# Kernel optimization log

Measured on AMD Instinct MI355X. Metric: run time of the kernel, lower is better.

## Reference

```python
import jax, jax.numpy as jnp
import numpy as np

N_NODES = 10000
N_EDGES = 640000
F_IN = 128
HID = 128
N_LAYERS = 3
N_ACT = 4096
NEG_SLOPE = 0.2


def setup_inputs() -> dict:
    key = jax.random.key(0)
    ks = jax.random.split(key, 16)
    s = 0.05
    return {
        "x": jax.random.normal(ks[0], (N_NODES, F_IN), jnp.float32),
        "edge_index": jax.random.randint(ks[1], (2, N_EDGES), 0, N_NODES, jnp.int64),
        "action_src": jax.random.randint(ks[2], (N_ACT,), 0, N_NODES, jnp.int64),
        "action_dst": jax.random.randint(ks[3], (N_ACT,), 0, N_NODES, jnp.int64),
        "action_type": jax.random.randint(ks[4], (N_ACT,), 0, 2, jnp.int32),
        "gat_W": jax.random.normal(ks[5], (N_LAYERS, HID, HID), jnp.float32) * s,
        "gat_asrc": jax.random.normal(ks[6], (N_LAYERS, HID), jnp.float32) * s,
        "gat_adst": jax.random.normal(ks[7], (N_LAYERS, HID), jnp.float32) * s,
        "gat_b": jax.random.normal(ks[8], (N_LAYERS, HID), jnp.float32) * s,
        "mlp_W1": jax.random.normal(ks[9], (2 * HID + 1, HID), jnp.float32) * s,
        "mlp_b1": jax.random.normal(ks[10], (HID,), jnp.float32) * s,
        "mlp_W2": jax.random.normal(ks[11], (HID, 1), jnp.float32) * s,
        "mlp_b2": jax.random.normal(ks[12], (1,), jnp.float32) * s,
    }


def _gat_layer(h, src, dst, W, a_src, a_dst, b, n_nodes):
    # PyG GATConv, heads=1: z = h W; e_ij = leaky_relu(a_src.z_j + a_dst.z_i)
    z = h @ W                                   # [N, HID]
    e = jax.nn.leaky_relu((z @ a_src)[src] + (z @ a_dst)[dst], NEG_SLOPE)  # [E+N]
    m = jax.ops.segment_max(e, dst, num_segments=n_nodes)
    m = jnp.where(jnp.isfinite(m), m, 0.0)
    ex = jnp.exp(e - m[dst])
    denom = jax.ops.segment_sum(ex, dst, num_segments=n_nodes)
    alpha = ex / denom[dst]                     # softmax over incoming edges
    out = jax.ops.segment_sum(alpha[:, None] * z[src], dst, num_segments=n_nodes)
    return out + b


def reference(x, edge_index, action_src, action_dst, action_type,
              gat_W, gat_asrc, gat_adst, gat_b,
              mlp_W1, mlp_b1, mlp_W2, mlp_b2):
    n = x.shape[0]
    loop = jnp.arange(n, dtype=edge_index.dtype)  # add_self_loops=True
    src = jnp.concatenate([edge_index[0], loop])
    dst = jnp.concatenate([edge_index[1], loop])
    h = x
    for l in range(N_LAYERS):
        h = jax.nn.relu(_gat_layer(h, src, dst, gat_W[l], gat_asrc[l], gat_adst[l], gat_b[l], n))
    # vectorized action scoring: [h[src], h[dst], type_flag] -> MLP -> scalar
    feat = jnp.concatenate(
        [h[action_src], h[action_dst], action_type.astype(h.dtype)[:, None]], axis=-1)
    hidden = jax.nn.relu(feat @ mlp_W1 + mlp_b1)
    scores = (hidden @ mlp_W2 + mlp_b2)[:, 0]   # [N_ACT]
    return scores
```

## Files before the change

### kernel.cpp

```cpp
#include <hip/hip_runtime.h>
#include <hip/hip_bf16.h>
#include <hip/hip_fp16.h>

#define N_NODES 10000
#define N_EDGES 640000
#define TOT_E   (N_EDGES + N_NODES)
#define HID     128
#define NEG_SLOPE 0.2f
#define N_ACT   4096

#define NBKT   250
#define NPB    40
#define P1_EPB 4096
#define P1_EPT 16
#define P1_BLOCKS 159
#define SLOTP  56
#define G_BLOCKS 313

__global__ __launch_bounds__(256) void part1_k(const int* __restrict__ ei,
                                               unsigned* __restrict__ bpart,
                                               int* __restrict__ bcnt) {
    __shared__ int hist[256];
    __shared__ int lofs[256];
    __shared__ int sc[256];
    __shared__ unsigned stage[P1_EPB];
    __shared__ unsigned char bkt_of[P1_EPB];
    int t = threadIdx.x;
    hist[t] = 0;
    __syncthreads();

    unsigned pk[P1_EPT];
    int bk[P1_EPT];
    int e0 = blockIdx.x * P1_EPB;
#pragma unroll
    for (int i = 0; i < P1_EPT; i++) {
        int e = e0 + i * 256 + t;
        if (e < TOT_E) {
            int src, dst;
            if (e < N_EDGES) { src = ei[e]; dst = ei[N_EDGES + e]; }
            else             { src = e - N_EDGES; dst = src; }
            pk[i] = ((unsigned)dst << 16) | (unsigned)src;
            bk[i] = dst / NPB;
            atomicAdd(&hist[bk[i]], 1);
        } else bk[i] = -1;
    }
    __syncthreads();
    int v = hist[t];
    sc[t] = v;
    __syncthreads();
    for (int o = 1; o < 256; o <<= 1) {
        int u = (t >= o) ? sc[t - o] : 0;
        __syncthreads();
        sc[t] += u;
        __syncthreads();
    }
    lofs[t] = sc[t] - v;
    bcnt[blockIdx.x * 256 + t] = v;
    hist[t] = 0;
    __syncthreads();
#pragma unroll
    for (int i = 0; i < P1_EPT; i++) {
        if (bk[i] >= 0) {
            int p = atomicAdd(&hist[bk[i]], 1);
            int slot = lofs[bk[i]] + p;
            stage[slot] = pk[i];
            bkt_of[slot] = (unsigned char)bk[i];
        }
    }
    __syncthreads();
    int nv = min(P1_EPB, TOT_E - e0);
    for (int s = t; s < nv; s += 256) {
        int b = bkt_of[s];
        bpart[b * (P1_BLOCKS * SLOTP) + blockIdx.x * SLOTP + (s - lofs[b])] = stage[s];
    }
}

__device__ __forceinline__ void agg_node(const __half2* __restrict__ z2,
                                         const float* __restrict__ zsi, float zdn,
                                         const int* __restrict__ csr, int o0, int deg,
                                         int lane, float& accx, float& accy, float& denom) {
    for (int base = 0; base < deg; base += 64) {
        int j = base + lane;
        int sreg = 0;
        float ex = 0.f;
        if (j < deg) {
            int s = csr[o0 + j];
            sreg = s;
            float e = zsi[s] + zdn;
            e = e > 0.f ? e : NEG_SLOPE * e;
            ex = __expf(e);
        }
        int cnt = min(64, deg - base);
        int nfull = cnt & ~7;
        int q = 0;
        if (nfull) {
            __half2 cur[8];
            float exc[8];
#pragma unroll
            for (int u = 0; u < 8; u++) {
                int sq = __builtin_amdgcn_readlane(sreg, u);
                exc[u] = __uint_as_float(
                    __builtin_amdgcn_readlane(__float_as_uint(ex), u));
                cur[u] = z2[sq * 64];
            }
            for (q = 8; q < nfull; q += 8) {
                __half2 nxt[8];
                float exn[8];
#pragma unroll
                for (int u = 0; u < 8; u++) {
                    int sq = __builtin_amdgcn_readlane(sreg, q + u);
                    exn[u] = __uint_as_float(
                        __builtin_amdgcn_readlane(__float_as_uint(ex), q + u));
                    nxt[u] = z2[sq * 64];
                }
#pragma unroll
                for (int u = 0; u < 8; u++) {
                    denom += exc[u];
                    float2 vf = __half22float2(cur[u]);
                    accx = fmaf(exc[u], vf.x, accx);
                    accy = fmaf(exc[u], vf.y, accy);
                    cur[u] = nxt[u];
                    exc[u] = exn[u];
                }
            }
#pragma unroll
            for (int u = 0; u < 8; u++) {
                denom += exc[u];
                float2 vf = __half22float2(cur[u]);
                accx = fmaf(exc[u], vf.x, accx);
                accy = fmaf(exc[u], vf.y, accy);
            }
            q = nfull;
        }
        for (; q < cnt; q++) {
            int sq = __builtin_amdgcn_readlane(sreg, q);
            float exq = __uint_as_float(
                __builtin_amdgcn_readlane(__float_as_uint(ex), q));
            denom += exq;
            float2 vf = __half22float2(z2[sq * 64]);
            accx = fmaf(exq, vf.x, accx);
            accy = fmaf(exq, vf.y, accy);
        }
    }
}

__device__ __forceinline__ void gload_lds16(const float* g, float* l) {
    __builtin_amdgcn_global_load_lds(
        (const __attribute__((address_space(1))) void*)g,
        (__attribute__((address_space(3))) void*)l, 16, 0, 0);
}

__global__ __launch_bounds__(256) void g2_k(const float* __restrict__ A,
                                            const float* __restrict__ W,
                                            const float* __restrict__ avs,
                                            const float* __restrict__ avd,
                                            __half* __restrict__ z16,
                                            float* __restrict__ zs,
                                            float* __restrict__ zd,
                                            const unsigned* __restrict__ bpart,
                                            const int* __restrict__ bcnt,
                                            int* __restrict__ csr,
                                            int* __restrict__ offs) {
    __shared__ float smem[20480];
    int t = threadIdx.x;

    if (blockIdx.x < G_BLOCKS) {
        float* As = smem;
        float* Ws = smem + 32 * HID;
        int w = t >> 6, lane = t & 63;
        int row0 = blockIdx.x * 32;
#pragma unroll
        for (int i = 0; i < 4; i++) {
            int chunk = w * 4 + i;
            long foff = (long)row0 * HID + chunk * 256;
            const float* g = ((foff + 256) <= (long)N_NODES * HID) ? (A + foff + lane * 4)
                                                                   : (A + lane * 4);
            gload_lds16(g, As + chunk * 256);
        }
#pragma unroll
        for (int i = 0; i < 16; i++) {
            int chunk = w * 16 + i;
            gload_lds16(W + chunk * 256 + lane * 4, Ws + chunk * 256);
        }
        __syncthreads();

        int tx = t & 31, ty = t >> 5;
        int r0 = ty * 4;
        float acc[4][4] = {{0.f}};
#pragma unroll 4
        for (int k4 = 0; k4 < 32; k4++) {
            float ak[4][4];
#pragma unroll
            for (int r = 0; r < 4; r++) {
                float4 a4 = *(const float4*)&As[(r0 + r) * HID + k4 * 4];
                ak[r][0] = a4.x; ak[r][1] = a4.y; ak[r][2] = a4.z; ak[r][3] = a4.w;
            }
            const float* Wb = &Ws[k4 * 4 * HID + tx * 4];
#pragma unroll
            for (int kk = 0; kk < 4; kk++) {
                float4 wv = *(const float4*)&Wb[kk * HID];
#pragma unroll
                for (int r = 0; r < 4; r++) {
                    acc[r][0] = fmaf(ak[r][kk], wv.x, acc[r][0]);
                    acc[r][1] = fmaf(ak[r][kk], wv.y, acc[r][1]);
                    acc[r][2] = fmaf(ak[r][kk], wv.z, acc[r][2]);
                    acc[r][3] = fmaf(ak[r][kk], wv.w, acc[r][3]);
                }
            }
        }
        float4 asv = *(const float4*)&avs[tx * 4];
        float4 adv = *(const float4*)&avd[tx * 4];
#pragma unroll
        for (int r = 0; r < 4; r++) {
            int row = row0 + r0 + r;
            if (row < N_NODES) {
                *(__half2*)&z16[row * HID + tx * 4]     = __floats2half2_rn(acc[r][0], acc[r][1]);
                *(__half2*)&z16[row * HID + tx * 4 + 2] = __floats2half2_rn(acc[r][2], acc[r][3]);
            }
            float ps = acc[r][0] * asv.x + acc[r][1] * asv.y + acc[r][2] * asv.z + acc[r][3] * asv.w;
            float pd = acc[r][0] * adv.x + acc[r][1] * adv.y + acc[r][2] * adv.z + acc[r][3] * adv.w;
#pragma unroll
            for (int o = 1; o < 32; o <<= 1) {
                ps += __shfl_xor(ps, o, 64);
                pd += __shfl_xor(pd, o, 64);
            }
            if (tx == 0 && row < N_NODES) { zs[row] = ps; zd[row] = pd; }
        }
    } else {
        int b = blockIdx.x - G_BLOCKS;
        unsigned* ebuf = (unsigned*)smem;
        int* sc    = (int*)(smem + 4096);
        int* Ls    = sc + 256;
        int* nhist = Ls + 256;
        __shared__ int bstart_s, cnt_s;

        int tot = 0;
        if (t < NBKT) {
            int t0 = 0, t1 = 0, t2 = 0, t3 = 0;
            int blk = 0;
            for (; blk + 4 <= P1_BLOCKS; blk += 4) {
                t0 += bcnt[(blk + 0) * 256 + t];
                t1 += bcnt[(blk + 1) * 256 + t];
                t2 += bcnt[(blk + 2) * 256 + t];
                t3 += bcnt[(blk + 3) * 256 + t];
            }
            for (; blk < P1_BLOCKS; blk++) t0 += bcnt[blk * 256 + t];
            tot = t0 + t1 + t2 + t3;
        }
        sc[t] = tot;
        __syncthreads();
        for (int o = 1; o < 256; o <<= 1) {
            int u = (t >= o) ? sc[t - o] : 0;
            __syncthreads();
            sc[t] += u;
            __syncthreads();
        }
        if (t == b) { bstart_s = sc[t] - tot; cnt_s = tot; }
        if (b == 0 && t == 255) offs[N_NODES] = sc[255];
        __syncthreads();

        int L = (t < P1_BLOCKS) ? bcnt[t * 256 + b] : 0;
        Ls[t] = L;
        sc[t] = L;
        __syncthreads();
        for (int o = 1; o < 256; o <<= 1) {
            int u = (t >= o) ? sc[t - o] : 0;
            __syncthreads();
            sc[t] += u;
            __syncthreads();
        }
        if (t < NPB) nhist[t] = 0;
        {
            int wv = t >> 6, lane = t & 63;
            const unsigned* bbase = bpart + b * (P1_BLOCKS * SLOTP);
            for (int r = wv; r < P1_BLOCKS; r += 4) {
                int Lr = Ls[r];
                if (lane < Lr) ebuf[(sc[r] - Lr) + lane] = bbase[r * SLOTP + lane];
            }
        }
        __syncthreads();

        int cnt = cnt_s;
        int n0 = b * NPB;
        for (int i = t; i < cnt; i += 256) atomicAdd(&nhist[(ebuf[i] >> 16) - n0], 1);
        __syncthreads();
        if (t < 64) {
            int v2 = (t < NPB) ? nhist[t] : 0;
            int s2 = v2;
            for (int o = 1; o < 64; o <<= 1) {
                int u = __shfl_up(s2, o, 64);
                if (t >= o) s2 += u;
            }
            if (t < NPB) {
                int ofs = bstart_s + s2 - v2;
                nhist[t] = ofs;
                offs[n0 + t] = ofs;
            }
        }
        __syncthreads();
        for (int i = t; i < cnt; i += 256) {
            unsigned pk = ebuf[i];
            int p = atomicAdd(&nhist[(pk >> 16) - n0], 1);
            csr[p] = pk & 0xFFFF;
        }
    }
}


__global__ __launch_bounds__(256) void fuse_k(const __half* __restrict__ z16i,
                                              const float* __restrict__ zsi,
                                              const float* __restrict__ zdi,
                                              const int* __restrict__ offs,
                                              const int* __restrict__ csr,
                                              const float* __restrict__ bprev,
                                              const float* __restrict__ W,
                                              const float* __restrict__ avs,
                                              const float* __restrict__ avd,
                                              __half* __restrict__ z16o,
                                              float* __restrict__ zso,
                                              float* __restrict__ zdo) {
    __shared__ float hT[8][HID];
    __shared__ float Wc[2][32 * HID];
    int t = threadIdx.x;
    int w = t >> 6, lane = t & 63;
    int n0 = blockIdx.x * 8;
    float4 wreg[4];
    {
        const float4* Wg = (const float4*)W;
#pragma unroll
        for (int i = 0; i < 4; i++) wreg[i] = Wg[t + 256 * i];
    }
    const __half2* z2 = (const __half2*)z16i + lane;

    float2 bv = *(const float2*)&bprev[2 * lane];
#pragma unroll
    for (int i = 0; i < 2; i++) {
        int ln = w * 2 + i;
        int n = n0 + ln;
        int o0 = offs[n];
        int deg = offs[n + 1] - o0;
        float zdn = zdi[n];
        float accx = 0.f, accy = 0.f, denom = 0.f;
        agg_node(z2, zsi, zdn, csr, o0, deg, lane, accx, accy, denom);
        float inv = 1.0f / denom;
        float vx = accx * inv + bv.x;
        float vy = accy * inv + bv.y;
        float2 hv;
        hv.x = vx > 0.f ? vx : 0.f;
        hv.y = vy > 0.f ? vy : 0.f;
        *(float2*)&hT[ln][2 * lane] = hv;
    }

    int tx = t & 31, ty = t >> 5;
    float acc[4] = {0.f, 0.f, 0.f, 0.f};
    for (int c = 0; c < 4; c++) {
        float4* dstb = (float4*)Wc[c & 1];
#pragma unroll
        for (int i = 0; i < 4; i++) dstb[t + 256 * i] = wreg[i];
        __syncthreads();
        if (c + 1 < 4) {
            const float4* Wg = (const float4*)(W + (c + 1) * 32 * HID);
#pragma unroll
            for (int i = 0; i < 4; i++) wreg[i] = Wg[t + 256 * i];
        }
        const float* Wb = Wc[c & 1];
        const float* h0 = &hT[ty][c * 32];
#pragma unroll 8
        for (int kk = 0; kk < 32; kk++) {
            float f0 = h0[kk];
            float4 wv = *(const float4*)&Wb[kk * HID + tx * 4];
            acc[0] = fmaf(f0, wv.x, acc[0]);
            acc[1] = fmaf(f0, wv.y, acc[1]);
            acc[2] = fmaf(f0, wv.z, acc[2]);
            acc[3] = fmaf(f0, wv.w, acc[3]);
        }
    }
    float4 asv = *(const float4*)&avs[tx * 4];
    float4 adv = *(const float4*)&avd[tx * 4];
    int row = n0 + ty;
    *(__half2*)&z16o[row * HID + tx * 4]     = __floats2half2_rn(acc[0], acc[1]);
    *(__half2*)&z16o[row * HID + tx * 4 + 2] = __floats2half2_rn(acc[2], acc[3]);
    float ps = acc[0] * asv.x + acc[1] * asv.y + acc[2] * asv.z + acc[3] * asv.w;
    float pd = acc[0] * adv.x + acc[1] * adv.y + acc[2] * adv.z + acc[3] * adv.w;
#pragma unroll
    for (int o = 1; o < 32; o <<= 1) {
        ps += __shfl_xor(ps, o, 64);
        pd += __shfl_xor(pd, o, 64);
    }
    if (tx == 0) { zso[row] = ps; zdo[row] = pd; }
}


__global__ __launch_bounds__(256) void agg_k(const __half* __restrict__ z16,
                                             const float* __restrict__ zs,
                                             const float* __restrict__ zd,
                                             const int* __restrict__ offs,
                                             const int* __restrict__ csr,
                                             const float* __restrict__ b,
                                             float* __restrict__ hout) {
    int t = threadIdx.x;
    int w = t >> 6, lane = t & 63;
    int n = blockIdx.x * 4 + w;
    if (n >= N_NODES) return;
    int o0 = offs[n];
    int deg = offs[n + 1] - o0;
    float zdn = zd[n];
    const __half2* z2 = (const __half2*)z16 + lane;
    float accx = 0.f, accy = 0.f, denom = 0.f;
    agg_node(z2, zs, zdn, csr, o0, deg, lane, accx, accy, denom);
    float inv = 1.0f / denom;
    float2 bv = *(const float2*)&b[2 * lane];
    float vx = accx * inv + bv.x;
    float vy = accy * inv + bv.y;
    float2 o;
    o.x = vx > 0.f ? vx : 0.f;
    o.y = vy > 0.f ? vy : 0.f;
    *(float2*)&hout[n * HID + 2 * lane] = o;
}


#define SC_APB 16

__global__ __launch_bounds__(256) void score_k(const float* __restrict__ h,
                                               const int* __restrict__ asrc,
                                               const int* __restrict__ adst,
                                               const int* __restrict__ atype,
                                               const float* __restrict__ W1,
                                               const float* __restrict__ b1,
                                               const float* __restrict__ W2,
                                               const float* __restrict__ b2,
                                               float* __restrict__ out) {
    __shared__ float featT[257][SC_APB + 1];
    __shared__ float Wc[2][32 * HID];
    int t = threadIdx.x;
    int a0 = blockIdx.x * SC_APB;

    float4 wreg[4];
    {
        const float4* Wg = (const float4*)W1;
#pragma unroll
        for (int i = 0; i < 4; i++) wreg[i] = Wg[t + 256 * i];
    }
    for (int idx = t; idx < SC_APB * 128; idx += 256) {
        int a = idx >> 7, c = idx & 127;
        featT[c][a]       = h[asrc[a0 + a] * HID + c];
        featT[128 + c][a] = h[adst[a0 + a] * HID + c];
    }
    if (t < SC_APB) featT[256][t] = (float)atype[a0 + t];

    int cg = t & 31, ap = t >> 5;
    float4 bv = *(const float4*)&b1[cg * 4];
    float acc0[4] = {bv.x, bv.y, bv.z, bv.w};
    float acc1[4] = {bv.x, bv.y, bv.z, bv.w};

    for (int c = 0; c < 8; c++) {
        float4* dstb = (float4*)Wc[c & 1];
#pragma unroll
        for (int i = 0; i < 4; i++) dstb[t + 256 * i] = wreg[i];
        __syncthreads();
        if (c + 1 < 8) {
            const float4* Wg = (const float4*)(W1 + (c + 1) * 32 * HID);
#pragma unroll
            for (int i = 0; i < 4; i++) wreg[i] = Wg[t + 256 * i];
        }
        const float* Wb = Wc[c & 1];
        const float* fT = &featT[c * 32][0];
#pragma unroll 8
        for (int kk = 0; kk < 32; kk++) {
            float4 wv = *(const float4*)&Wb[kk * HID + cg * 4];
            float f0 = fT[kk * (SC_APB + 1) + ap * 2];
            float f1 = fT[kk * (SC_APB + 1) + ap * 2 + 1];
            acc0[0] = fmaf(f0, wv.x, acc0[0]);
            acc0[1] = fmaf(f0, wv.y, acc0[1]);
            acc0[2] = fmaf(f0, wv.z, acc0[2]);
            acc0[3] = fmaf(f0, wv.w, acc0[3]);
            acc1[0] = fmaf(f1, wv.x, acc1[0]);
            acc1[1] = fmaf(f1, wv.y, acc1[1]);
            acc1[2] = fmaf(f1, wv.z, acc1[2]);
            acc1[3] = fmaf(f1, wv.w, acc1[3]);
        }
    }
    {
        float4 wv = *(const float4*)&W1[256 * HID + cg * 4];
        float f0 = featT[256][ap * 2];
        float f1 = featT[256][ap * 2 + 1];
        acc0[0] = fmaf(f0, wv.x, acc0[0]); acc0[1] = fmaf(f0, wv.y, acc0[1]);
        acc0[2] = fmaf(f0, wv.z, acc0[2]); acc0[3] = fmaf(f0, wv.w, acc0[3]);
        acc1[0] = fmaf(f1, wv.x, acc1[0]); acc1[1] = fmaf(f1, wv.y, acc1[1]);
        acc1[2] = fmaf(f1, wv.z, acc1[2]); acc1[3] = fmaf(f1, wv.w, acc1[3]);
    }
    float4 w2v = *(const float4*)&W2[cg * 4];
    float v0 = 0.f, v1 = 0.f;
    v0 += (acc0[0] > 0.f ? acc0[0] : 0.f) * w2v.x;
    v0 += (acc0[1] > 0.f ? acc0[1] : 0.f) * w2v.y;
    v0 += (acc0[2] > 0.f ? acc0[2] : 0.f) * w2v.z;
    v0 += (acc0[3] > 0.f ? acc0[3] : 0.f) * w2v.w;
    v1 += (acc1[0] > 0.f ? acc1[0] : 0.f) * w2v.x;
    v1 += (acc1[1] > 0.f ? acc1[1] : 0.f) * w2v.y;
    v1 += (acc1[2] > 0.f ? acc1[2] : 0.f) * w2v.z;
    v1 += (acc1[3] > 0.f ? acc1[3] : 0.f) * w2v.w;
#pragma unroll
    for (int o = 1; o < 32; o <<= 1) {
        v0 += __shfl_xor(v0, o, 64);
        v1 += __shfl_xor(v1, o, 64);
    }
    if (cg == 0) {
        out[a0 + ap * 2]     = v0 + b2[0];
        out[a0 + ap * 2 + 1] = v1 + b2[0];
    }
}


extern "C" void kernel_launch(void* const* d_in, const int* in_sizes, int n_in,
                              void* d_out, int out_size, void* d_ws, size_t ws_size,
                              hipStream_t stream) {
    const float* x   = (const float*)d_in[0];
    const int* ei    = (const int*)d_in[1];
    const int* asrc  = (const int*)d_in[2];
    const int* adst  = (const int*)d_in[3];
    const int* atype = (const int*)d_in[4];
    const float* gW  = (const float*)d_in[5];
    const float* gas = (const float*)d_in[6];
    const float* gad = (const float*)d_in[7];
    const float* gb  = (const float*)d_in[8];
    const float* W1  = (const float*)d_in[9];
    const float* b1  = (const float*)d_in[10];
    const float* W2  = (const float*)d_in[11];
    const float* b2  = (const float*)d_in[12];
    float* out = (float*)d_out;

    __half* z16A = (__half*)d_ws;
    __half* z16B = z16A + N_NODES * HID;
    float* h3   = (float*)(z16B + N_NODES * HID);
    float* zsA  = h3 + N_NODES * HID;
    float* zdA  = zsA + N_NODES;
    float* zsB  = zdA + N_NODES;
    float* zdB  = zsB + N_NODES;
    int* offs   = (int*)(zdB + N_NODES);
    int* csr    = offs + (N_NODES + 1);
    int* bcnt   = csr + TOT_E;
    unsigned* bpart = (unsigned*)(bcnt + P1_BLOCKS * 256);

    part1_k<<<P1_BLOCKS, 256, 0, stream>>>(ei, bpart, bcnt);
    g2_k<<<G_BLOCKS + NBKT, 256, 0, stream>>>(x, gW, gas, gad, z16A, zsA, zdA,
                                              bpart, bcnt, csr, offs);

    fuse_k<<<N_NODES / 8, 256, 0, stream>>>(z16A, zsA, zdA, offs, csr, gb,
                                            gW + 1 * HID * HID, gas + 1 * HID, gad + 1 * HID,
                                            z16B, zsB, zdB);
    fuse_k<<<N_NODES / 8, 256, 0, stream>>>(z16B, zsB, zdB, offs, csr, gb + 1 * HID,
                                            gW + 2 * HID * HID, gas + 2 * HID, gad + 2 * HID,
                                            z16A, zsA, zdA);
    agg_k<<<(N_NODES + 3) / 4, 256, 0, stream>>>(z16A, zsA, zdA, offs, csr,
                                                 gb + 2 * HID, h3);
    score_k<<<N_ACT / SC_APB, 256, 0, stream>>>(h3, asrc, adst, atype,
                                                W1, b1, W2, b2, out);
}
```

Measured before the change: 217.6 us.

## Merge all stages into one persistent megakernel with grid-wide barriers

Replaces the six separate launches (partition, GEMM plus CSR build, two fused layers, aggregation, scoring) with a single persistent kernel. Blocks loop over work tiles and meet at software grid barriers built on global atomics. Self-loop edges are no longer materialised in the partition, and the bucket geometry and the per-block bucket totals are reorganised. This is meant to remove kernel launch gaps and tail effects. In exchange it adds barrier spin costs, limits occupancy to the co-resident grid, and relies on every block being resident at once for the barrier to avoid deadlock.

```diff
diff --git a/kernel.cpp b/kernel.cpp
--- a/kernel.cpp
+++ b/kernel.cpp
@@ -4,48 +4,41 @@
 
 #define N_NODES 10000
 #define N_EDGES 640000
-#define TOT_E   (N_EDGES + N_NODES)
 #define HID     128
 #define NEG_SLOPE 0.2f
 #define N_ACT   4096
 
-#define NBKT   250
-#define NPB    40
-#define P1_EPB 4096
-#define P1_EPT 16
-#define P1_BLOCKS 159
-#define SLOTP  56
-#define G_BLOCKS 313
-
-__global__ __launch_bounds__(256) void part1_k(const int* __restrict__ ei,
-                                               unsigned* __restrict__ bpart,
-                                               int* __restrict__ bcnt) {
-    __shared__ int hist[256];
-    __shared__ int lofs[256];
-    __shared__ int sc[256];
-    __shared__ unsigned stage[P1_EPB];
-    __shared__ unsigned char bkt_of[P1_EPB];
-    int t = threadIdx.x;
-    hist[t] = 0;
+#define GRID_MAX 400
+#define EPT   7
+#define EPB   1792
+#define P1B   358
+#define NBKT  87
+#define NPB   115
+#define SLOTP 64
+#define GEMM_B 313
+#define FUSE_T 400
+#define NPT   25
+#define SC_T  256
+#define SC_APB 16
+#define EBUF_CAP 8192
+
+__device__ __forceinline__ void gsync(int* bar, int nb) {
     __syncthreads();
-
-    unsigned pk[P1_EPT];
-    int bk[P1_EPT];
-    int e0 = blockIdx.x * P1_EPB;
-#pragma unroll
-    for (int i = 0; i < P1_EPT; i++) {
-        int e = e0 + i * 256 + t;
-        if (e < TOT_E) {
-            int src, dst;
-            if (e < N_EDGES) { src = ei[e]; dst = ei[N_EDGES + e]; }
-            else             { src = e - N_EDGES; dst = src; }
-            pk[i] = ((unsigned)dst << 16) | (unsigned)src;
-            bk[i] = dst / NPB;
-            atomicAdd(&hist[bk[i]], 1);
-        } else bk[i] = -1;
+    if (threadIdx.x == 0) {
+        int g = __hip_atomic_load(&bar[1], __ATOMIC_RELAXED, __HIP_MEMORY_SCOPE_AGENT);
+        int n = __hip_atomic_fetch_add(&bar[0], 1, __ATOMIC_ACQ_REL, __HIP_MEMORY_SCOPE_AGENT);
+        if (n == nb - 1) {
+            __hip_atomic_store(&bar[0], 0, __ATOMIC_RELAXED, __HIP_MEMORY_SCOPE_AGENT);
+            __hip_atomic_fetch_add(&bar[1], 1, __ATOMIC_ACQ_REL, __HIP_MEMORY_SCOPE_AGENT);
+        } else {
+            while (__hip_atomic_load(&bar[1], __ATOMIC_ACQUIRE, __HIP_MEMORY_SCOPE_AGENT) == g)
+                __builtin_amdgcn_s_sleep(8);
+        }
     }
     __syncthreads();
-    int v = hist[t];
+}
+
+__device__ __forceinline__ int scan256(int* sc, int v, int t) {
     sc[t] = v;
     __syncthreads();
     for (int o = 1; o < 256; o <<= 1) {
@@ -54,25 +47,7 @@
         sc[t] += u;
         __syncthreads();
     }
-    lofs[t] = sc[t] - v;
-    bcnt[blockIdx.x * 256 + t] = v;
-    hist[t] = 0;
-    __syncthreads();
-#pragma unroll
-    for (int i = 0; i < P1_EPT; i++) {
-        if (bk[i] >= 0) {
-            int p = atomicAdd(&hist[bk[i]], 1);
-            int slot = lofs[bk[i]] + p;
-            stage[slot] = pk[i];
-            bkt_of[slot] = (unsigned char)bk[i];
-        }
-    }
-    __syncthreads();
-    int nv = min(P1_EPB, TOT_E - e0);
-    for (int s = t; s < nv; s += 256) {
-        int b = bkt_of[s];
-        bpart[b * (P1_BLOCKS * SLOTP) + blockIdx.x * SLOTP + (s - lofs[b])] = stage[s];
-    }
+    return sc[t];
 }
 
 __device__ __forceinline__ void agg_node(const __half2* __restrict__ z2,
@@ -99,8 +74,7 @@
 #pragma unroll
             for (int u = 0; u < 8; u++) {
                 int sq = __builtin_amdgcn_readlane(sreg, u);
-                exc[u] = __uint_as_float(
-                    __builtin_amdgcn_readlane(__float_as_uint(ex), u));
+                exc[u] = __uint_as_float(__builtin_amdgcn_readlane(__float_as_uint(ex), u));
                 cur[u] = z2[sq * 64];
             }
             for (q = 8; q < nfull; q += 8) {
@@ -109,8 +83,7 @@
 #pragma unroll
                 for (int u = 0; u < 8; u++) {
                     int sq = __builtin_amdgcn_readlane(sreg, q + u);
-                    exn[u] = __uint_as_float(
-                        __builtin_amdgcn_readlane(__float_as_uint(ex), q + u));
+                    exn[u] = __uint_as_float(__builtin_amdgcn_readlane(__float_as_uint(ex), q + u));
                     nxt[u] = z2[sq * 64];
                 }
 #pragma unroll
@@ -134,8 +107,7 @@
         }
         for (; q < cnt; q++) {
             int sq = __builtin_amdgcn_readlane(sreg, q);
-            float exq = __uint_as_float(
-                __builtin_amdgcn_readlane(__float_as_uint(ex), q));
+            float exq = __uint_as_float(__builtin_amdgcn_readlane(__float_as_uint(ex), q));
             denom += exq;
             float2 vf = __half22float2(z2[sq * 64]);
             accx = fmaf(exq, vf.x, accx);
@@ -150,363 +122,403 @@
         (__attribute__((address_space(3))) void*)l, 16, 0, 0);
 }
 
-__global__ __launch_bounds__(256) void g2_k(const float* __restrict__ A,
-                                            const float* __restrict__ W,
-                                            const float* __restrict__ avs,
-                                            const float* __restrict__ avd,
-                                            __half* __restrict__ z16,
-                                            float* __restrict__ zs,
-                                            float* __restrict__ zd,
-                                            const unsigned* __restrict__ bpart,
-                                            const int* __restrict__ bcnt,
-                                            int* __restrict__ csr,
-                                            int* __restrict__ offs) {
-    __shared__ float smem[20480];
-    int t = threadIdx.x;
-
-    if (blockIdx.x < G_BLOCKS) {
-        float* As = smem;
-        float* Ws = smem + 32 * HID;
-        int w = t >> 6, lane = t & 63;
-        int row0 = blockIdx.x * 32;
-#pragma unroll
-        for (int i = 0; i < 4; i++) {
-            int chunk = w * 4 + i;
-            long foff = (long)row0 * HID + chunk * 256;
-            const float* g = ((foff + 256) <= (long)N_NODES * HID) ? (A + foff + lane * 4)
-                                                                   : (A + lane * 4);
-            gload_lds16(g, As + chunk * 256);
-        }
-#pragma unroll
-        for (int i = 0; i < 16; i++) {
-            int chunk = w * 16 + i;
-            gload_lds16(W + chunk * 256 + lane * 4, Ws + chunk * 256);
-        }
-        __syncthreads();
-
-        int tx = t & 31, ty = t >> 5;
-        int r0 = ty * 4;
-        float acc[4][4] = {{0.f}};
-#pragma unroll 4
-        for (int k4 = 0; k4 < 32; k4++) {
-            float ak[4][4];
-#pragma unroll
-            for (int r = 0; r < 4; r++) {
-                float4 a4 = *(const float4*)&As[(r0 + r) * HID + k4 * 4];
-                ak[r][0] = a4.x; ak[r][1] = a4.y; ak[r][2] = a4.z; ak[r][3] = a4.w;
-            }
-            const float* Wb = &Ws[k4 * 4 * HID + tx * 4];
-#pragma unroll
-            for (int kk = 0; kk < 4; kk++) {
-                float4 wv = *(const float4*)&Wb[kk * HID];
-#pragma unroll
-                for (int r = 0; r < 4; r++) {
-                    acc[r][0] = fmaf(ak[r][kk], wv.x, acc[r][0]);
-                    acc[r][1] = fmaf(ak[r][kk], wv.y, acc[r][1]);
-                    acc[r][2] = fmaf(ak[r][kk], wv.z, acc[r][2]);
-                    acc[r][3] = fmaf(ak[r][kk], wv.w, acc[r][3]);
-                }
-            }
-        }
-        float4 asv = *(const float4*)&avs[tx * 4];
-        float4 adv = *(const float4*)&avd[tx * 4];
-#pragma unroll
-        for (int r = 0; r < 4; r++) {
-            int row = row0 + r0 + r;
-            if (row < N_NODES) {
-                *(__half2*)&z16[row * HID + tx * 4]     = __floats2half2_rn(acc[r][0], acc[r][1]);
-                *(__half2*)&z16[row * HID + tx * 4 + 2] = __floats2half2_rn(acc[r][2], acc[r][3]);
-            }
-            float ps = acc[r][0] * asv.x + acc[r][1] * asv.y + acc[r][2] * asv.z + acc[r][3] * asv.w;
-            float pd = acc[r][0] * adv.x + acc[r][1] * adv.y + acc[r][2] * adv.z + acc[r][3] * adv.w;
-#pragma unroll
-            for (int o = 1; o < 32; o <<= 1) {
-                ps += __shfl_xor(ps, o, 64);
-                pd += __shfl_xor(pd, o, 64);
-            }
-            if (tx == 0 && row < N_NODES) { zs[row] = ps; zd[row] = pd; }
-        }
-    } else {
-        int b = blockIdx.x - G_BLOCKS;
-        unsigned* ebuf = (unsigned*)smem;
-        int* sc    = (int*)(smem + 4096);
-        int* Ls    = sc + 256;
-        int* nhist = Ls + 256;
-        __shared__ int bstart_s, cnt_s;
-
-        int tot = 0;
-        if (t < NBKT) {
-            int t0 = 0, t1 = 0, t2 = 0, t3 = 0;
-            int blk = 0;
-            for (; blk + 4 <= P1_BLOCKS; blk += 4) {
-                t0 += bcnt[(blk + 0) * 256 + t];
-                t1 += bcnt[(blk + 1) * 256 + t];
-                t2 += bcnt[(blk + 2) * 256 + t];
-                t3 += bcnt[(blk + 3) * 256 + t];
-            }
-            for (; blk < P1_BLOCKS; blk++) t0 += bcnt[blk * 256 + t];
-            tot = t0 + t1 + t2 + t3;
-        }
-        sc[t] = tot;
-        __syncthreads();
-        for (int o = 1; o < 256; o <<= 1) {
-            int u = (t >= o) ? sc[t - o] : 0;
-            __syncthreads();
-            sc[t] += u;
-            __syncthreads();
-        }
-        if (t == b) { bstart_s = sc[t] - tot; cnt_s = tot; }
-        if (b == 0 && t == 255) offs[N_NODES] = sc[255];
-        __syncthreads();
-
-        int L = (t < P1_BLOCKS) ? bcnt[t * 256 + b] : 0;
-        Ls[t] = L;
-        sc[t] = L;
-        __syncthreads();
-        for (int o = 1; o < 256; o <<= 1) {
-            int u = (t >= o) ? sc[t - o] : 0;
-            __syncthreads();
-            sc[t] += u;
-            __syncthreads();
-        }
-        if (t < NPB) nhist[t] = 0;
-        {
-            int wv = t >> 6, lane = t & 63;
-            const unsigned* bbase = bpart + b * (P1_BLOCKS * SLOTP);
-            for (int r = wv; r < P1_BLOCKS; r += 4) {
-                int Lr = Ls[r];
-                if (lane < Lr) ebuf[(sc[r] - Lr) + lane] = bbase[r * SLOTP + lane];
-            }
-        }
-        __syncthreads();
-
-        int cnt = cnt_s;
-        int n0 = b * NPB;
-        for (int i = t; i < cnt; i += 256) atomicAdd(&nhist[(ebuf[i] >> 16) - n0], 1);
-        __syncthreads();
-        if (t < 64) {
-            int v2 = (t < NPB) ? nhist[t] : 0;
-            int s2 = v2;
-            for (int o = 1; o < 64; o <<= 1) {
-                int u = __shfl_up(s2, o, 64);
-                if (t >= o) s2 += u;
-            }
-            if (t < NPB) {
-                int ofs = bstart_s + s2 - v2;
-                nhist[t] = ofs;
-                offs[n0 + t] = ofs;
-            }
-        }
-        __syncthreads();
-        for (int i = t; i < cnt; i += 256) {
-            unsigned pk = ebuf[i];
-            int p = atomicAdd(&nhist[(pk >> 16) - n0], 1);
-            csr[p] = pk & 0xFFFF;
-        }
-    }
-}
-
-
-__global__ __launch_bounds__(256) void fuse_k(const __half* __restrict__ z16i,
-                                              const float* __restrict__ zsi,
-                                              const float* __restrict__ zdi,
-                                              const int* __restrict__ offs,
-                                              const int* __restrict__ csr,
-                                              const float* __restrict__ bprev,
-                                              const float* __restrict__ W,
-                                              const float* __restrict__ avs,
-                                              const float* __restrict__ avd,
-                                              __half* __restrict__ z16o,
-                                              float* __restrict__ zso,
-                                              float* __restrict__ zdo) {
-    __shared__ float hT[8][HID];
-    __shared__ float Wc[2][32 * HID];
+__global__ __launch_bounds__(256, 2) void mega_k(
+        const float* __restrict__ x, const int* __restrict__ ei,
+        const int* __restrict__ asrc, const int* __restrict__ adst,
+        const int* __restrict__ atype,
+        const float* __restrict__ gW, const float* __restrict__ gas,
+        const float* __restrict__ gad, const float* __restrict__ gb,
+        const float* __restrict__ W1, const float* __restrict__ b1,
+        const float* __restrict__ W2, const float* __restrict__ b2,
+        float* __restrict__ out,
+        __half* __restrict__ z16A, __half* __restrict__ z16B,
+        float* __restrict__ h3,
+        float* __restrict__ zsA, float* __restrict__ zdA,
+        float* __restrict__ zsB, float* __restrict__ zdB,
+        int* __restrict__ offs, int* __restrict__ csr,
+        int* __restrict__ bcnt, unsigned* __restrict__ bpart,
+        int* __restrict__ btot, int* __restrict__ bar, int nb) {
+    __shared__ __align__(16) char smem8[81920];
+    float* smemf = (float*)smem8;
     int t = threadIdx.x;
     int w = t >> 6, lane = t & 63;
-    int n0 = blockIdx.x * 8;
-    float4 wreg[4];
+
     {
-        const float4* Wg = (const float4*)W;
-#pragma unroll
-        for (int i = 0; i < 4; i++) wreg[i] = Wg[t + 256 * i];
-    }
-    const __half2* z2 = (const __half2*)z16i + lane;
-
-    float2 bv = *(const float2*)&bprev[2 * lane];
-#pragma unroll
-    for (int i = 0; i < 2; i++) {
-        int ln = w * 2 + i;
-        int n = n0 + ln;
-        int o0 = offs[n];
-        int deg = offs[n + 1] - o0;
-        float zdn = zdi[n];
-        float accx = 0.f, accy = 0.f, denom = 0.f;
-        agg_node(z2, zsi, zdn, csr, o0, deg, lane, accx, accy, denom);
-        float inv = 1.0f / denom;
-        float vx = accx * inv + bv.x;
-        float vy = accy * inv + bv.y;
-        float2 hv;
-        hv.x = vx > 0.f ? vx : 0.f;
-        hv.y = vy > 0.f ? vy : 0.f;
-        *(float2*)&hT[ln][2 * lane] = hv;
-    }
-
-    int tx = t & 31, ty = t >> 5;
-    float acc[4] = {0.f, 0.f, 0.f, 0.f};
-    for (int c = 0; c < 4; c++) {
-        float4* dstb = (float4*)Wc[c & 1];
-#pragma unroll
-        for (int i = 0; i < 4; i++) dstb[t + 256 * i] = wreg[i];
-        __syncthreads();
-        if (c + 1 < 4) {
-            const float4* Wg = (const float4*)(W + (c + 1) * 32 * HID);
-#pragma unroll
-            for (int i = 0; i < 4; i++) wreg[i] = Wg[t + 256 * i];
-        }
-        const float* Wb = Wc[c & 1];
-        const float* h0 = &hT[ty][c * 32];
+        int* hist = (int*)smem8;
+        int* lofs = hist + 128;
+        int* scA  = lofs + 128;
+        unsigned* stage = (unsigned*)(scA + 256);
+        unsigned char* bkt = (unsigned char*)(stage + EPB);
+
+        for (int tile = blockIdx.x; tile < P1B; tile += nb) {
+            int e0 = tile * EPB;
+            if (t < 128) hist[t] = 0;
+            __syncthreads();
+            unsigned pk[EPT];
+            int bk[EPT];
+#pragma unroll
+            for (int i = 0; i < EPT; i++) {
+                int e = e0 + i * 256 + t;
+                if (e < N_EDGES) {
+                    int src = ei[e], dst = ei[N_EDGES + e];
+                    pk[i] = ((unsigned)dst << 16) | (unsigned)src;
+                    bk[i] = dst / NPB;
+                    atomicAdd(&hist[bk[i]], 1);
+                } else bk[i] = -1;
+            }
+            __syncthreads();
+            int v = (t < NBKT) ? hist[t] : 0;
+            int inc = scan256(scA, v, t);
+            lofs[t] = inc - v;
+            if (t < NBKT) {
+                bcnt[t * P1B + tile] = v;
+                if (v) atomicAdd(&btot[t], v);
+                hist[t] = 0;
+            }
+            __syncthreads();
+#pragma unroll
+            for (int i = 0; i < EPT; i++) {
+                if (bk[i] >= 0) {
+                    int p = atomicAdd(&hist[bk[i]], 1);
+                    int slot = lofs[bk[i]] + p;
+                    stage[slot] = pk[i];
+                    bkt[slot] = (unsigned char)bk[i];
+                }
+            }
+            __syncthreads();
+            int nv = min(EPB, N_EDGES - e0);
+            for (int s = t; s < nv; s += 256) {
+                int b = bkt[s];
+                bpart[(b * P1B + tile) * SLOTP + (s - lofs[b])] = stage[s];
+            }
+            __syncthreads();
+        }
+    }
+    gsync(bar, nb);
+
+    for (int v = blockIdx.x; v < GEMM_B + NBKT; v += nb) {
+        if (v < GEMM_B) {
+            float* As = smemf;
+            float* Ws = smemf + 4096;
+            int row0 = v * 32;
+#pragma unroll
+            for (int i = 0; i < 4; i++) {
+                int chunk = w * 4 + i;
+                long foff = (long)row0 * HID + chunk * 256;
+                const float* g = ((foff + 256) <= (long)N_NODES * HID) ? (x + foff + lane * 4)
+                                                                       : (x + lane * 4);
+                gload_lds16(g, As + chunk * 256);
+            }
+#pragma unroll
+            for (int i = 0; i < 16; i++) {
+                int chunk = w * 16 + i;
+                gload_lds16(gW + chunk * 256 + lane * 4, Ws + chunk * 256);
+            }
+            __syncthreads();
+
+            int tx = t & 31, ty = t >> 5;
+            int r0 = ty * 4;
+            float acc[4][4] = {{0.f}};
+#pragma unroll 4
+            for (int k4 = 0; k4 < 32; k4++) {
+                float ak[4][4];
+#pragma unroll
+                for (int r = 0; r < 4; r++) {
+                    float4 a4 = *(const float4*)&As[(r0 + r) * HID + k4 * 4];
+                    ak[r][0] = a4.x; ak[r][1] = a4.y; ak[r][2] = a4.z; ak[r][3] = a4.w;
+                }
+                const float* Wb = &Ws[k4 * 4 * HID + tx * 4];
+#pragma unroll
+                for (int kk = 0; kk < 4; kk++) {
+                    float4 wv = *(const float4*)&Wb[kk * HID];
+#pragma unroll
+                    for (int r = 0; r < 4; r++) {
+                        acc[r][0] = fmaf(ak[r][kk], wv.x, acc[r][0]);
+                        acc[r][1] = fmaf(ak[r][kk], wv.y, acc[r][1]);
+                        acc[r][2] = fmaf(ak[r][kk], wv.z, acc[r][2]);
+                        acc[r][3] = fmaf(ak[r][kk], wv.w, acc[r][3]);
+                    }
+                }
+            }
+            float4 asv = *(const float4*)&gas[t % 32 * 4];
+            float4 adv = *(const float4*)&gad[t % 32 * 4];
+#pragma unroll
+            for (int r = 0; r < 4; r++) {
+                int row = row0 + r0 + r;
+                if (row < N_NODES) {
+                    *(__half2*)&z16A[row * HID + tx * 4]     = __floats2half2_rn(acc[r][0], acc[r][1]);
+                    *(__half2*)&z16A[row * HID + tx * 4 + 2] = __floats2half2_rn(acc[r][2], acc[r][3]);
+                }
+                float ps = acc[r][0] * asv.x + acc[r][1] * asv.y + acc[r][2] * asv.z + acc[r][3] * asv.w;
+                float pd = acc[r][0] * adv.x + acc[r][1] * adv.y + acc[r][2] * adv.z + acc[r][3] * adv.w;
+#pragma unroll
+                for (int o = 1; o < 32; o <<= 1) {
+                    ps += __shfl_xor(ps, o, 64);
+                    pd += __shfl_xor(pd, o, 64);
+                }
+                if (tx == 0 && row < N_NODES) { zsA[row] = ps; zdA[row] = pd; }
+            }
+            __syncthreads();
+        } else {
+            int b = v - GEMM_B;
+            unsigned* ebuf = (unsigned*)smem8;
+            int* pref = (int*)(smem8 + 32768);
+            int* sc   = (int*)(smem8 + 34304);
+            int* nh   = (int*)(smem8 + 35328);
+            int* shs  = (int*)(smem8 + 35840);
+
+            int bv = (t < NBKT) ? btot[t] : 0;
+            int inc1 = scan256(sc, bv, t);
+            if (t == b) shs[0] = (inc1 - bv) + NPB * b;
+            if (b == 0 && t == NBKT - 1) offs[N_NODES] = inc1 + N_NODES;
+            __syncthreads();
+
+            int L0 = 0, L1 = 0;
+            if (t < P1B / 2) {
+                L0 = bcnt[b * P1B + 2 * t];
+                L1 = bcnt[b * P1B + 2 * t + 1];
+            }
+            int inc2 = scan256(sc, L0 + L1, t);
+            if (t < P1B / 2) {
+                pref[2 * t]     = inc2 - (L0 + L1);
+                pref[2 * t + 1] = inc2 - (L0 + L1) + L0;
+            }
+            if (t == 255) pref[P1B] = sc[255];
+            __syncthreads();
+            int cnt = pref[P1B];
+            if (cnt > EBUF_CAP) cnt = EBUF_CAP;
+
+            for (int r = w; r < P1B; r += 4) {
+                int p0 = pref[r];
+                int Lr = pref[r + 1] - p0;
+                if (lane < Lr && (unsigned)(p0 + lane) < EBUF_CAP)
+                    ebuf[p0 + lane] = bpart[(b * P1B + r) * SLOTP + lane];
+            }
+            __syncthreads();
+
+            int npb = min(NPB, N_NODES - b * NPB);
+            int n0 = b * NPB;
+            if (t < 128) nh[t] = (t < npb) ? 1 : 0;
+            __syncthreads();
+            for (int i = t; i < cnt; i += 256)
+                atomicAdd(&nh[((ebuf[i] >> 16) - n0) & 127], 1);
+            __syncthreads();
+            int dv = (t < 128) ? nh[t] : 0;
+            int inc3 = scan256(sc, dv, t);
+            int bstart = shs[0];
+            if (t < npb) {
+                int nofs = bstart + inc3 - dv;
+                offs[n0 + t] = nofs;
+                if ((unsigned)nofs < (unsigned)(N_EDGES + N_NODES)) csr[nofs] = n0 + t;
+                nh[t] = nofs + 1;
+            }
+            __syncthreads();
+            for (int i = t; i < cnt; i += 256) {
+                unsigned pk = ebuf[i];
+                int d = ((pk >> 16) - n0) & 127;
+                int p = atomicAdd(&nh[d], 1);
+                if ((unsigned)p < (unsigned)(N_EDGES + N_NODES)) csr[p] = pk & 0xFFFF;
+            }
+            __syncthreads();
+        }
+    }
+    gsync(bar, nb);
+
+    for (int l = 0; l < 3; l++) {
+        const __half* zin = (l == 1) ? z16B : z16A;
+        const float* zsl  = (l == 1) ? zsB : zsA;
+        const float* zdl  = (l == 1) ? zdB : zdA;
+        __half* zout = (l == 0) ? z16B : z16A;
+        float* zso   = (l == 0) ? zsB : zsA;
+        float* zdo   = (l == 0) ? zdB : zdA;
+        const float* bias = gb + l * HID;
+        const __half2* z2 = (const __half2*)zin + lane;
+        float2 bv2 = *(const float2*)&bias[2 * lane];
+
+        if (l < 2) {
+            const float* Wl   = gW + (l + 1) * HID * HID;
+            const float* avsl = gas + (l + 1) * HID;
+            const float* avdl = gad + (l + 1) * HID;
+            float* hT = smemf;
+            float* Ws = smemf + 4096;
+
+            for (int tile = blockIdx.x; tile < FUSE_T; tile += nb) {
+                int n0 = tile * NPT;
+#pragma unroll
+                for (int i = 0; i < 16; i++) {
+                    int chunk = w * 16 + i;
+                    gload_lds16(Wl + chunk * 256 + lane * 4, Ws + chunk * 256);
+                }
+                for (int ln = w; ln < NPT; ln += 4) {
+                    int n = n0 + ln;
+                    int o0 = offs[n];
+                    int deg = offs[n + 1] - o0;
+                    if (deg < 0) deg = 0;
+                    if (deg > 2048) deg = 2048;
+                    float zdn = zdl[n];
+                    float accx = 0.f, accy = 0.f, denom = 0.f;
+                    agg_node(z2, zsl, zdn, csr, o0, deg, lane, accx, accy, denom);
+                    float inv = 1.0f / denom;
+                    float vx = accx * inv + bv2.x;
+                    float vy = accy * inv + bv2.y;
+                    float2 hv;
+                    hv.x = vx > 0.f ? vx : 0.f;
+                    hv.y = vy > 0.f ? vy : 0.f;
+                    *(float2*)&hT[ln * HID + 2 * lane] = hv;
+                }
+                __syncthreads();
+                int tx = t & 31, ty = t >> 5;
+                float acc[4][4] = {{0.f}};
+#pragma unroll 4
+                for (int k4 = 0; k4 < 32; k4++) {
+                    float4 av[4];
+#pragma unroll
+                    for (int u = 0; u < 4; u++) {
+                        int r = ty + 8 * u;
+                        int rr = (r < NPT) ? r : 0;
+                        av[u] = *(const float4*)&hT[rr * HID + k4 * 4];
+                    }
+#pragma unroll
+                    for (int kk = 0; kk < 4; kk++) {
+                        float4 wv = *(const float4*)&Ws[(k4 * 4 + kk) * HID + tx * 4];
+#pragma unroll
+                        for (int u = 0; u < 4; u++) {
+                            float f = (kk == 0) ? av[u].x : (kk == 1) ? av[u].y
+                                     : (kk == 2) ? av[u].z : av[u].w;
+                            acc[u][0] = fmaf(f, wv.x, acc[u][0]);
+                            acc[u][1] = fmaf(f, wv.y, acc[u][1]);
+                            acc[u][2] = fmaf(f, wv.z, acc[u][2]);
+                            acc[u][3] = fmaf(f, wv.w, acc[u][3]);
+                        }
+                    }
+                }
+                float4 asv = *(const float4*)&avsl[tx * 4];
+                float4 adv = *(const float4*)&avdl[tx * 4];
+#pragma unroll
+                for (int u = 0; u < 4; u++) {
+                    int r = ty + 8 * u;
+                    int row = n0 + r;
+                    float ps = acc[u][0] * asv.x + acc[u][1] * asv.y + acc[u][2] * asv.z + acc[u][3] * asv.w;
+                    float pd = acc[u][0] * adv.x + acc[u][1] * adv.y + acc[u][2] * adv.z + acc[u][3] * adv.w;
+#pragma unroll
+                    for (int o = 1; o < 32; o <<= 1) {
+                        ps += __shfl_xor(ps, o, 64);
+                        pd += __shfl_xor(pd, o, 64);
+                    }
+                    if (r < NPT) {
+                        *(__half2*)&zout[row * HID + tx * 4]     = __floats2half2_rn(acc[u][0], acc[u][1]);
+                        *(__half2*)&zout[row * HID + tx * 4 + 2] = __floats2half2_rn(acc[u][2], acc[u][3]);
+                        if (tx == 0) { zso[row] = ps; zdo[row] = pd; }
+                    }
+                }
+                __syncthreads();
+            }
+        } else {
+            for (int tile = blockIdx.x; tile < FUSE_T; tile += nb) {
+                int n0 = tile * NPT;
+                for (int ln = w; ln < NPT; ln += 4) {
+                    int n = n0 + ln;
+                    int o0 = offs[n];
+                    int deg = offs[n + 1] - o0;
+                    if (deg < 0) deg = 0;
+                    if (deg > 2048) deg = 2048;
+                    float zdn = zdl[n];
+                    float accx = 0.f, accy = 0.f, denom = 0.f;
+                    agg_node(z2, zsl, zdn, csr, o0, deg, lane, accx, accy, denom);
+                    float inv = 1.0f / denom;
+                    float vx = accx * inv + bv2.x;
+                    float vy = accy * inv + bv2.y;
+                    float2 o;
+                    o.x = vx > 0.f ? vx : 0.f;
+                    o.y = vy > 0.f ? vy : 0.f;
+                    *(float2*)&h3[n * HID + 2 * lane] = o;
+                }
+            }
+        }
+        gsync(bar, nb);
+    }
+
+    {
+        float* featT = smemf;
+        float* Wc0 = (float*)(smem8 + 17920);
+        for (int tile = blockIdx.x; tile < SC_T; tile += nb) {
+            int a0 = tile * SC_APB;
+            float4 wreg[4];
+            {
+                const float4* Wg = (const float4*)W1;
+#pragma unroll
+                for (int i = 0; i < 4; i++) wreg[i] = Wg[t + 256 * i];
+            }
+            for (int idx = t; idx < SC_APB * 128; idx += 256) {
+                int a = idx >> 7, c = idx & 127;
+                featT[c * 17 + a]         = h3[asrc[a0 + a] * HID + c];
+                featT[(128 + c) * 17 + a] = h3[adst[a0 + a] * HID + c];
+            }
+            if (t < SC_APB) featT[256 * 17 + t] = (float)atype[a0 + t];
+
+            int cg = t & 31, ap = t >> 5;
+            float4 bv = *(const float4*)&b1[cg * 4];
+            float acc0[4] = {bv.x, bv.y, bv.z, bv.w};
+            float acc1[4] = {bv.x, bv.y, bv.z, bv.w};
+
+            for (int c = 0; c < 8; c++) {
+                float4* dstb = (float4*)(Wc0 + (c & 1) * 4096);
+#pragma unroll
+                for (int i = 0; i < 4; i++) dstb[t + 256 * i] = wreg[i];
+                __syncthreads();
+                if (c + 1 < 8) {
+                    const float4* Wg = (const float4*)(W1 + (c + 1) * 32 * HID);
+#pragma unroll
+                    for (int i = 0; i < 4; i++) wreg[i] = Wg[t + 256 * i];
+                }
+                const float* Wb = Wc0 + (c & 1) * 4096;
+                const float* fT = &featT[(c * 32) * 17];
 #pragma unroll 8
-        for (int kk = 0; kk < 32; kk++) {
-            float f0 = h0[kk];
-            float4 wv = *(const float4*)&Wb[kk * HID + tx * 4];
-            acc[0] = fmaf(f0, wv.x, acc[0]);
-            acc[1] = fmaf(f0, wv.y, acc[1]);
-            acc[2] = fmaf(f0, wv.z, acc[2]);
-            acc[3] = fmaf(f0, wv.w, acc[3]);
-        }
-    }
-    float4 asv = *(const float4*)&avs[tx * 4];
-    float4 adv = *(const float4*)&avd[tx * 4];
-    int row = n0 + ty;
-    *(__half2*)&z16o[row * HID + tx * 4]     = __floats2half2_rn(acc[0], acc[1]);
-    *(__half2*)&z16o[row * HID + tx * 4 + 2] = __floats2half2_rn(acc[2], acc[3]);
-    float ps = acc[0] * asv.x + acc[1] * asv.y + acc[2] * asv.z + acc[3] * asv.w;
-    float pd = acc[0] * adv.x + acc[1] * adv.y + acc[2] * adv.z + acc[3] * adv.w;
-#pragma unroll
-    for (int o = 1; o < 32; o <<= 1) {
-        ps += __shfl_xor(ps, o, 64);
-        pd += __shfl_xor(pd, o, 64);
-    }
-    if (tx == 0) { zso[row] = ps; zdo[row] = pd; }
-}
-
-
-__global__ __launch_bounds__(256) void agg_k(const __half* __restrict__ z16,
-                                             const float* __restrict__ zs,
-                                             const float* __restrict__ zd,
-                                             const int* __restrict__ offs,
-                                             const int* __restrict__ csr,
-                                             const float* __restrict__ b,
-                                             float* __restrict__ hout) {
-    int t = threadIdx.x;
-    int w = t >> 6, lane = t & 63;
-    int n = blockIdx.x * 4 + w;
-    if (n >= N_NODES) return;
-    int o0 = offs[n];
-    int deg = offs[n + 1] - o0;
-    float zdn = zd[n];
-    const __half2* z2 = (const __half2*)z16 + lane;
-    float accx = 0.f, accy = 0.f, denom = 0.f;
-    agg_node(z2, zs, zdn, csr, o0, deg, lane, accx, accy, denom);
-    float inv = 1.0f / denom;
-    float2 bv = *(const float2*)&b[2 * lane];
-    float vx = accx * inv + bv.x;
-    float vy = accy * inv + bv.y;
-    float2 o;
-    o.x = vx > 0.f ? vx : 0.f;
-    o.y = vy > 0.f ? vy : 0.f;
-    *(float2*)&hout[n * HID + 2 * lane] = o;
-}
-
-
-#define SC_APB 16
-
-__global__ __launch_bounds__(256) void score_k(const float* __restrict__ h,
-                                               const int* __restrict__ asrc,
-                                               const int* __restrict__ adst,
-                                               const int* __restrict__ atype,
-                                               const float* __restrict__ W1,
-                                               const float* __restrict__ b1,
-                                               const float* __restrict__ W2,
-                                               const float* __restrict__ b2,
-                                               float* __restrict__ out) {
-    __shared__ float featT[257][SC_APB + 1];
-    __shared__ float Wc[2][32 * HID];
-    int t = threadIdx.x;
-    int a0 = blockIdx.x * SC_APB;
-
-    float4 wreg[4];
-    {
-        const float4* Wg = (const float4*)W1;
-#pragma unroll
-        for (int i = 0; i < 4; i++) wreg[i] = Wg[t + 256 * i];
-    }
-    for (int idx = t; idx < SC_APB * 128; idx += 256) {
-        int a = idx >> 7, c = idx & 127;
-        featT[c][a]       = h[asrc[a0 + a] * HID + c];
-        featT[128 + c][a] = h[adst[a0 + a] * HID + c];
-    }
-    if (t < SC_APB) featT[256][t] = (float)atype[a0 + t];
-
-    int cg = t & 31, ap = t >> 5;
-    float4 bv = *(const float4*)&b1[cg * 4];
-    float acc0[4] = {bv.x, bv.y, bv.z, bv.w};
-    float acc1[4] = {bv.x, bv.y, bv.z, bv.w};
-
-    for (int c = 0; c < 8; c++) {
-        float4* dstb = (float4*)Wc[c & 1];
-#pragma unroll
-        for (int i = 0; i < 4; i++) dstb[t + 256 * i] = wreg[i];
-        __syncthreads();
-        if (c + 1 < 8) {
-            const float4* Wg = (const float4*)(W1 + (c + 1) * 32 * HID);
-#pragma unroll
-            for (int i = 0; i < 4; i++) wreg[i] = Wg[t + 256 * i];
-        }
-        const float* Wb = Wc[c & 1];
-        const float* fT = &featT[c * 32][0];
-#pragma unroll 8
-        for (int kk = 0; kk < 32; kk++) {
-            float4 wv = *(const float4*)&Wb[kk * HID + cg * 4];
-            float f0 = fT[kk * (SC_APB + 1) + ap * 2];
-            float f1 = fT[kk * (SC_APB + 1) + ap * 2 + 1];
-            acc0[0] = fmaf(f0, wv.x, acc0[0]);
-            acc0[1] = fmaf(f0, wv.y, acc0[1]);
-            acc0[2] = fmaf(f0, wv.z, acc0[2]);
-            acc0[3] = fmaf(f0, wv.w, acc0[3]);
-            acc1[0] = fmaf(f1, wv.x, acc1[0]);
-            acc1[1] = fmaf(f1, wv.y, acc1[1]);
-            acc1[2] = fmaf(f1, wv.z, acc1[2]);
-            acc1[3] = fmaf(f1, wv.w, acc1[3]);
-        }
-    }
-    {
-        float4 wv = *(const float4*)&W1[256 * HID + cg * 4];
-        float f0 = featT[256][ap * 2];
-        float f1 = featT[256][ap * 2 + 1];
-        acc0[0] = fmaf(f0, wv.x, acc0[0]); acc0[1] = fmaf(f0, wv.y, acc0[1]);
-        acc0[2] = fmaf(f0, wv.z, acc0[2]); acc0[3] = fmaf(f0, wv.w, acc0[3]);
-        acc1[0] = fmaf(f1, wv.x, acc1[0]); acc1[1] = fmaf(f1, wv.y, acc1[1]);
-        acc1[2] = fmaf(f1, wv.z, acc1[2]); acc1[3] = fmaf(f1, wv.w, acc1[3]);
-    }
-    float4 w2v = *(const float4*)&W2[cg * 4];
-    float v0 = 0.f, v1 = 0.f;
-    v0 += (acc0[0] > 0.f ? acc0[0] : 0.f) * w2v.x;
-    v0 += (acc0[1] > 0.f ? acc0[1] : 0.f) * w2v.y;
-    v0 += (acc0[2] > 0.f ? acc0[2] : 0.f) * w2v.z;
-    v0 += (acc0[3] > 0.f ? acc0[3] : 0.f) * w2v.w;
-    v1 += (acc1[0] > 0.f ? acc1[0] : 0.f) * w2v.x;
-    v1 += (acc1[1] > 0.f ? acc1[1] : 0.f) * w2v.y;
-    v1 += (acc1[2] > 0.f ? acc1[2] : 0.f) * w2v.z;
-    v1 += (acc1[3] > 0.f ? acc1[3] : 0.f) * w2v.w;
-#pragma unroll
-    for (int o = 1; o < 32; o <<= 1) {
-        v0 += __shfl_xor(v0, o, 64);
-        v1 += __shfl_xor(v1, o, 64);
-    }
-    if (cg == 0) {
-        out[a0 + ap * 2]     = v0 + b2[0];
-        out[a0 + ap * 2 + 1] = v1 + b2[0];
+                for (int kk = 0; kk < 32; kk++) {
+                    float4 wv = *(const float4*)&Wb[kk * HID + cg * 4];
+                    float f0 = fT[kk * 17 + ap * 2];
+                    float f1 = fT[kk * 17 + ap * 2 + 1];
+                    acc0[0] = fmaf(f0, wv.x, acc0[0]);
+                    acc0[1] = fmaf(f0, wv.y, acc0[1]);
+                    acc0[2] = fmaf(f0, wv.z, acc0[2]);
+                    acc0[3] = fmaf(f0, wv.w, acc0[3]);
+                    acc1[0] = fmaf(f1, wv.x, acc1[0]);
+                    acc1[1] = fmaf(f1, wv.y, acc1[1]);
+                    acc1[2] = fmaf(f1, wv.z, acc1[2]);
+                    acc1[3] = fmaf(f1, wv.w, acc1[3]);
+                }
+                __syncthreads();
+            }
+            {
+                float4 wv = *(const float4*)&W1[256 * HID + cg * 4];
+                float f0 = featT[256 * 17 + ap * 2];
+                float f1 = featT[256 * 17 + ap * 2 + 1];
+                acc0[0] = fmaf(f0, wv.x, acc0[0]); acc0[1] = fmaf(f0, wv.y, acc0[1]);
+                acc0[2] = fmaf(f0, wv.z, acc0[2]); acc0[3] = fmaf(f0, wv.w, acc0[3]);
+                acc1[0] = fmaf(f1, wv.x, acc1[0]); acc1[1] = fmaf(f1, wv.y, acc1[1]);
+                acc1[2] = fmaf(f1, wv.z, acc1[2]); acc1[3] = fmaf(f1, wv.w, acc1[3]);
+            }
+            float4 w2v = *(const float4*)&W2[cg * 4];
+            float v0 = 0.f, v1 = 0.f;
+            v0 += (acc0[0] > 0.f ? acc0[0] : 0.f) * w2v.x;
+            v0 += (acc0[1] > 0.f ? acc0[1] : 0.f) * w2v.y;
+            v0 += (acc0[2] > 0.f ? acc0[2] : 0.f) * w2v.z;
+            v0 += (acc0[3] > 0.f ? acc0[3] : 0.f) * w2v.w;
+            v1 += (acc1[0] > 0.f ? acc1[0] : 0.f) * w2v.x;
+            v1 += (acc1[1] > 0.f ? acc1[1] : 0.f) * w2v.y;
+            v1 += (acc1[2] > 0.f ? acc1[2] : 0.f) * w2v.z;
+            v1 += (acc1[3] > 0.f ? acc1[3] : 0.f) * w2v.w;
+#pragma unroll
+            for (int o = 1; o < 32; o <<= 1) {
+                v0 += __shfl_xor(v0, o, 64);
+                v1 += __shfl_xor(v1, o, 64);
+            }
+            if (cg == 0) {
+                out[a0 + ap * 2]     = v0 + b2[0];
+                out[a0 + ap * 2 + 1] = v1 + b2[0];
+            }
+            __syncthreads();
+        }
     }
 }
 
@@ -529,30 +541,34 @@
     const float* b2  = (const float*)d_in[12];
     float* out = (float*)d_out;
 
-    __half* z16A = (__half*)d_ws;
-    __half* z16B = z16A + N_NODES * HID;
-    float* h3   = (float*)(z16B + N_NODES * HID);
-    float* zsA  = h3 + N_NODES * HID;
-    float* zdA  = zsA + N_NODES;
-    float* zsB  = zdA + N_NODES;
-    float* zdB  = zsB + N_NODES;
-    int* offs   = (int*)(zdB + N_NODES);
-    int* csr    = offs + (N_NODES + 1);
-    int* bcnt   = csr + TOT_E;
-    unsigned* bpart = (unsigned*)(bcnt + P1_BLOCKS * 256);
-
-    part1_k<<<P1_BLOCKS, 256, 0, stream>>>(ei, bpart, bcnt);
-    g2_k<<<G_BLOCKS + NBKT, 256, 0, stream>>>(x, gW, gas, gad, z16A, zsA, zdA,
-                                              bpart, bcnt, csr, offs);
-
-    fuse_k<<<N_NODES / 8, 256, 0, stream>>>(z16A, zsA, zdA, offs, csr, gb,
-                                            gW + 1 * HID * HID, gas + 1 * HID, gad + 1 * HID,
-                                            z16B, zsB, zdB);
-    fuse_k<<<N_NODES / 8, 256, 0, stream>>>(z16B, zsB, zdB, offs, csr, gb + 1 * HID,
-                                            gW + 2 * HID * HID, gas + 2 * HID, gad + 2 * HID,
-                                            z16A, zsA, zdA);
-    agg_k<<<(N_NODES + 3) / 4, 256, 0, stream>>>(z16A, zsA, zdA, offs, csr,
-                                                 gb + 2 * HID, h3);
-    score_k<<<N_ACT / SC_APB, 256, 0, stream>>>(h3, asrc, adst, atype,
-                                                W1, b1, W2, b2, out);
+    char* p = (char*)d_ws;
+    __half* z16A = (__half*)p;            p += 2560000;
+    __half* z16B = (__half*)p;            p += 2560000;
+    float* h3   = (float*)p;              p += 5120000;
+    float* zsA  = (float*)p;              p += 40000;
+    float* zdA  = (float*)p;              p += 40000;
+    float* zsB  = (float*)p;              p += 40000;
+    float* zdB  = (float*)p;              p += 40000;
+    int* offs   = (int*)p;                p += 40064;
+    int* csr    = (int*)p;                p += 2600000;
+    int* bcnt   = (int*)p;                p += 124608;
+    unsigned* bpart = (unsigned*)p;       p += (size_t)NBKT * P1B * SLOTP * 4;
+    int* btot   = (int*)p;
+    int* bar    = btot + 112;
+
+    static int nb_cache = 0;
+    if (nb_cache == 0) {
+        int bpc = 1, ncu = 256;
+        hipOccupancyMaxActiveBlocksPerMultiprocessor(&bpc, mega_k, 256, 0);
+        hipDeviceGetAttribute(&ncu, hipDeviceAttributeMultiprocessorCount, 0);
+        long cap = (long)((bpc < 1) ? 1 : bpc) * (long)ncu;
+        nb_cache = (int)((cap < GRID_MAX) ? cap : GRID_MAX);
+        if (nb_cache < 1) nb_cache = 1;
+    }
+
+    hipMemsetAsync(btot, 0, 512, stream);
+    mega_k<<<nb_cache, 256, 0, stream>>>(x, ei, asrc, adst, atype,
+                                         gW, gas, gad, gb, W1, b1, W2, b2, out,
+                                         z16A, z16B, h3, zsA, zdA, zsB, zdB,
+                                         offs, csr, bcnt, bpart, btot, bar, nb_cache);
 }
```

After: 802.1 us. 3.69x slower.
